# Performance work log

Hardware: AMD Instinct MI355X
Metric: run time of the kernel (lower is better)

## Reference

```python
import jax, jax.numpy as jnp
import numpy as np
import math

HEAD = 4
B, N, C = 8, 1024, 256


def setup_inputs() -> dict:
    key = jax.random.key(0)
    k1, k2, k3, k4, k5 = jax.random.split(key, 5)
    query = jax.random.normal(k1, (B, N, C), dtype=jnp.float32)
    keyt = jax.random.normal(k2, (B, N, C), dtype=jnp.float32)
    value = jax.random.normal(k3, (B, N, C), dtype=jnp.float32)
    mask = jax.random.randint(k4, (B, N, N), 0, 2).astype(bool)
    dis = jax.random.normal(k5, (B, N, N), dtype=jnp.float32)
    return {"query": query, "key": keyt, "value": value, "mask": mask, "dis": dis}


def reference(query, key, value, mask, dis):
    Bq, Nq, Cq = key.shape
    d = Cq // HEAD
    # split heads: [B,N,C] -> [h,B,N,d]
    q = query.reshape(Bq, Nq, HEAD, d).transpose(2, 0, 1, 3)
    k = key.reshape(Bq, Nq, HEAD, d).transpose(2, 0, 1, 3)
    v = value.reshape(Bq, Nq, HEAD, d).transpose(2, 0, 1, 3)
    # scores: [h,B,N,N]; note: dis added BEFORE scaling, as in the torch code
    scores = jnp.einsum('hbnd,hbmd->hbnm', q, k)
    scores = scores + dis[None]            # dis broadcasts over head dim
    scores = scores / math.sqrt(d)
    scores = jnp.where(mask[None], -jnp.inf, scores)
    p_attn = jax.nn.softmax(scores, axis=-1)
    out = jnp.einsum('hbnm,hbmd->hbnd', p_attn, v)  # [h,B,N,d]
    out = out.transpose(1, 2, 0, 3).reshape(Bq, Nq, Cq)
    return out, p_attn
```

## Files before the change

kernel.cpp:

```cpp
#include <hip/hip_runtime.h>
#include <math.h>

#define HEADS 4
#define BATCH 8
#define SEQ   1024
#define CH    256
#define DH    64
#define RB    16
#define MC    64
#define NTHR  256
#define SSTR  1032

typedef float  floatx4  __attribute__((ext_vector_type(4)));
typedef short  shortx8  __attribute__((ext_vector_type(8)));
typedef unsigned short ushortx4 __attribute__((ext_vector_type(4)));

__device__ __forceinline__ unsigned short f2bf(float f) {
    unsigned u = __float_as_uint(f);
    unsigned r = u + 0x7FFFu + ((u >> 16) & 1u);
    return (unsigned short)(r >> 16);
}
__device__ __forceinline__ float bf2f(unsigned short h) {
    return __uint_as_float(((unsigned)h) << 16);
}
__device__ __forceinline__ shortx8 pack8(float4 a, float4 b) {
    shortx8 r;
    r[0] = (short)f2bf(a.x); r[1] = (short)f2bf(a.y);
    r[2] = (short)f2bf(a.z); r[3] = (short)f2bf(a.w);
    r[4] = (short)f2bf(b.x); r[5] = (short)f2bf(b.y);
    r[6] = (short)f2bf(b.z); r[7] = (short)f2bf(b.w);
    return r;
}

__global__ void detect_mask_kernel(const unsigned char* __restrict__ mb,
                                   int* __restrict__ flag) {
    int t = threadIdx.x;
    int found = 0;
    for (int o = t * 64; o < t * 64 + 64; ++o)
        if ((o & 3) != 0 && mb[o] != 0) found = 1;
    unsigned long long ball = __ballot(found != 0);
    if (t == 0) flag[0] = (ball != 0ULL) ? 1 : 0;
}

__global__ __launch_bounds__(NTHR, 4)
void attn_mfma(const float* __restrict__ q, const float* __restrict__ k,
               const float* __restrict__ v, const void* __restrict__ maskp,
               const float* __restrict__ dis, float* __restrict__ out,
               float* __restrict__ pout, const int* __restrict__ flag)
{
    __shared__ unsigned short Sraw[RB][SSTR];
    __shared__ float invs[RB];

    const int t   = threadIdx.x;
    const int bid = blockIdx.x;
    const int nb  = bid & 63;
    const int hb  = bid >> 6;
    const int b   = hb & (BATCH - 1);
    const int h   = hb >> 3;
    const int n0  = nb * RB;
    const int fl  = flag[0];
    const unsigned char* mask8  = (const unsigned char*)maskp;
    const int*           mask32 = (const int*)maskp;

    const int lane = t & 63;
    const int w    = t >> 6;
    const int ln   = lane & 15;
    const int qd   = lane >> 4;

    const float* qrow = q + ((size_t)(b * SEQ + n0 + ln)) * CH + h * DH;
    shortx8 aq0, aq1;
    {
        float4 a0 = *(const float4*)(qrow + qd * 8);
        float4 a1 = *(const float4*)(qrow + qd * 8 + 4);
        float4 a2 = *(const float4*)(qrow + 32 + qd * 8);
        float4 a3 = *(const float4*)(qrow + 32 + qd * 8 + 4);
        aq0 = pack8(a0, a1);
        aq1 = pack8(a2, a3);
    }

    const float* kbase = k + ((size_t)(b * SEQ)) * CH + h * DH;
    const float* vbase = v + ((size_t)(b * SEQ)) * CH + h * DH;

    for (int mc = 0; mc < SEQ / MC; ++mc) {
        const int mg = mc * MC + w * 16 + ln;
        const float* krow = kbase + (size_t)mg * CH;
        float4 k0 = *(const float4*)(krow + qd * 8);
        float4 k1 = *(const float4*)(krow + qd * 8 + 4);
        float4 k2 = *(const float4*)(krow + 32 + qd * 8);
        float4 k3 = *(const float4*)(krow + 32 + qd * 8 + 4);
        const size_t dibase = ((size_t)(b * SEQ + n0 + qd * 4)) * SEQ + mg;
        float dv[4]; int mk[4];
        if (fl) {
            #pragma unroll
            for (int r = 0; r < 4; ++r) mk[r] = mask8[dibase + (size_t)r * SEQ];
        } else {
            #pragma unroll
            for (int r = 0; r < 4; ++r) mk[r] = mask32[dibase + (size_t)r * SEQ];
        }
        #pragma unroll
        for (int r = 0; r < 4; ++r) dv[r] = dis[dibase + (size_t)r * SEQ];

        shortx8 b0 = pack8(k0, k1), b1 = pack8(k2, k3);
        floatx4 acc = {0.f, 0.f, 0.f, 0.f};
        acc = __builtin_amdgcn_mfma_f32_16x16x32_bf16(aq0, b0, acc, 0, 0, 0);
        acc = __builtin_amdgcn_mfma_f32_16x16x32_bf16(aq1, b1, acc, 0, 0, 0);
        #pragma unroll
        for (int r = 0; r < 4; ++r) {
            float sc = mk[r] ? -INFINITY : (acc[r] + dv[r]) * 0.125f;
            Sraw[qd * 4 + r][mg] = f2bf(sc);
        }
    }
    __syncthreads();

    {
        const int r = t >> 4, l = t & 15;
        float mx = -INFINITY;
        #pragma unroll
        for (int j = 0; j < 8; ++j) {
            shortx8 sv = *(const shortx8*)&Sraw[r][j * 128 + l * 8];
            #pragma unroll
            for (int e = 0; e < 8; ++e) mx = fmaxf(mx, bf2f((unsigned short)sv[e]));
        }
        #pragma unroll
        for (int off = 8; off; off >>= 1) mx = fmaxf(mx, __shfl_xor(mx, off, 16));
        float sum = 0.f;
        #pragma unroll
        for (int j = 0; j < 8; ++j) {
            shortx8 sv = *(const shortx8*)&Sraw[r][j * 128 + l * 8];
            shortx8 ev;
            #pragma unroll
            for (int e = 0; e < 8; ++e) {
                float x = __expf(bf2f((unsigned short)sv[e]) - mx);
                sum += x;
                ev[e] = (short)f2bf(x);
            }
            *(shortx8*)&Sraw[r][j * 128 + l * 8] = ev;
        }
        #pragma unroll
        for (int off = 8; off; off >>= 1) sum += __shfl_xor(sum, off, 16);
        if (l == 0) invs[r] = 1.0f / sum;
    }
    __syncthreads();

    {
        float* prow = pout + ((size_t)((h * BATCH + b) * SEQ + n0)) * SEQ;
        #pragma unroll
        for (int i = 0; i < RB; ++i) {
            const float inv = invs[i];
            ushortx4 sp = *(const ushortx4*)&Sraw[i][t * 4];
            float4 pv = { bf2f(sp[0]) * inv, bf2f(sp[1]) * inv,
                          bf2f(sp[2]) * inv, bf2f(sp[3]) * inv };
            *(float4*)(prow + (size_t)i * SEQ + t * 4) = pv;
        }
    }

    floatx4 acco = {0.f, 0.f, 0.f, 0.f};
    for (int mc = 0; mc < SEQ / MC; ++mc) {
        #pragma unroll
        for (int s = 0; s < 2; ++s) {
            const int kb = mc * MC + s * 32 + qd * 8;
            float vv[8];
            #pragma unroll
            for (int j = 0; j < 8; ++j)
                vv[j] = vbase[(size_t)(kb + j) * CH + w * 16 + ln];
            shortx8 af = *(const shortx8*)&Sraw[ln][mc * MC + s * 32 + qd * 8];
            shortx8 bfv;
            #pragma unroll
            for (int j = 0; j < 8; ++j) bfv[j] = (short)f2bf(vv[j]);
            acco = __builtin_amdgcn_mfma_f32_16x16x32_bf16(af, bfv, acco, 0, 0, 0);
        }
    }
    #pragma unroll
    for (int r = 0; r < 4; ++r) {
        int row = qd * 4 + r;
        out[((size_t)(b * SEQ + n0 + row)) * CH + h * DH + w * 16 + ln]
            = acco[r] * invs[row];
    }
}

extern "C" void kernel_launch(void* const* d_in, const int* in_sizes, int n_in,
                              void* d_out, int out_size, void* d_ws, size_t ws_size,
                              hipStream_t stream) {
    const float* q    = (const float*)d_in[0];
    const float* k    = (const float*)d_in[1];
    const float* v    = (const float*)d_in[2];
    const void*  mask = d_in[3];
    const float* dis  = (const float*)d_in[4];
    float* out  = (float*)d_out;
    float* pout = out + (size_t)BATCH * SEQ * CH;
    int*   flag = (int*)d_ws;

    detect_mask_kernel<<<1, 64, 0, stream>>>((const unsigned char*)mask, flag);
    attn_mfma<<<HEADS * BATCH * (SEQ / RB), NTHR, 0, stream>>>(
        q, k, v, mask, dis, out, pout, flag);
}
```

Before: 315.1 us.

## Double threads per block, split PV over key halves, inline mask detection

Raises the block size from 256 to 512 threads. The score loop now covers 128 keys per iteration with 8 waves, and the softmax uses 32 lanes per row. The P@V stage splits the key range in half across two groups of waves, and the partial outputs are reduced through shared memory. The separate mask-format detection kernel is removed: each block samples the mask itself with a ballot, which saves a launch at the cost of a small redundant read in every block. The extra shared buffer and the higher launch-bounds target may limit occupancy or registers.

```diff
diff --git a/kernel.cpp b/kernel.cpp
--- a/kernel.cpp
+++ b/kernel.cpp
@@ -7,13 +7,11 @@
 #define CH    256
 #define DH    64
 #define RB    16
-#define MC    64
-#define NTHR  256
+#define NTHR  512
 #define SSTR  1032
 
 typedef float  floatx4  __attribute__((ext_vector_type(4)));
 typedef short  shortx8  __attribute__((ext_vector_type(8)));
-typedef unsigned short ushortx4 __attribute__((ext_vector_type(4)));
 
 __device__ __forceinline__ unsigned short f2bf(float f) {
     unsigned u = __float_as_uint(f);
@@ -32,23 +30,14 @@
     return r;
 }
 
-__global__ void detect_mask_kernel(const unsigned char* __restrict__ mb,
-                                   int* __restrict__ flag) {
-    int t = threadIdx.x;
-    int found = 0;
-    for (int o = t * 64; o < t * 64 + 64; ++o)
-        if ((o & 3) != 0 && mb[o] != 0) found = 1;
-    unsigned long long ball = __ballot(found != 0);
-    if (t == 0) flag[0] = (ball != 0ULL) ? 1 : 0;
-}
-
-__global__ __launch_bounds__(NTHR, 4)
+__global__ __launch_bounds__(NTHR, 8)
 void attn_mfma(const float* __restrict__ q, const float* __restrict__ k,
                const float* __restrict__ v, const void* __restrict__ maskp,
                const float* __restrict__ dis, float* __restrict__ out,
-               float* __restrict__ pout, const int* __restrict__ flag)
+               float* __restrict__ pout)
 {
     __shared__ unsigned short Sraw[RB][SSTR];
+    __shared__ float Opart[RB][65];
     __shared__ float invs[RB];
 
     const int t   = threadIdx.x;
@@ -58,14 +47,23 @@
     const int b   = hb & (BATCH - 1);
     const int h   = hb >> 3;
     const int n0  = nb * RB;
-    const int fl  = flag[0];
-    const unsigned char* mask8  = (const unsigned char*)maskp;
-    const int*           mask32 = (const int*)maskp;
 
     const int lane = t & 63;
     const int w    = t >> 6;
     const int ln   = lane & 15;
     const int qd   = lane >> 4;
+
+    int fl;
+    {
+        const unsigned* mw = (const unsigned*)maskp;
+        int found = 0;
+        #pragma unroll
+        for (int j = 0; j < 16; ++j)
+            if (mw[lane * 16 + j] & 0xFFFFFF00u) found = 1;
+        fl = (__ballot(found != 0) != 0ULL) ? 1 : 0;
+    }
+    const unsigned char* mask8  = (const unsigned char*)maskp;
+    const int*           mask32 = (const int*)maskp;
 
     const float* qrow = q + ((size_t)(b * SEQ + n0 + ln)) * CH + h * DH;
     shortx8 aq0, aq1;
@@ -81,24 +79,25 @@
     const float* kbase = k + ((size_t)(b * SEQ)) * CH + h * DH;
     const float* vbase = v + ((size_t)(b * SEQ)) * CH + h * DH;
 
-    for (int mc = 0; mc < SEQ / MC; ++mc) {
-        const int mg = mc * MC + w * 16 + ln;
+    #pragma unroll 2
+    for (int mc = 0; mc < 8; ++mc) {
+        const int mg = mc * 128 + w * 16 + ln;
+        const size_t dibase = ((size_t)(b * SEQ + n0 + qd * 4)) * SEQ + mg;
+        float dv[4]; int mk[4];
+        #pragma unroll
+        for (int r = 0; r < 4; ++r) dv[r] = dis[dibase + (size_t)r * SEQ];
+        if (fl) {
+            #pragma unroll
+            for (int r = 0; r < 4; ++r) mk[r] = mask8[dibase + (size_t)r * SEQ];
+        } else {
+            #pragma unroll
+            for (int r = 0; r < 4; ++r) mk[r] = mask32[dibase + (size_t)r * SEQ];
+        }
         const float* krow = kbase + (size_t)mg * CH;
         float4 k0 = *(const float4*)(krow + qd * 8);
         float4 k1 = *(const float4*)(krow + qd * 8 + 4);
         float4 k2 = *(const float4*)(krow + 32 + qd * 8);
         float4 k3 = *(const float4*)(krow + 32 + qd * 8 + 4);
-        const size_t dibase = ((size_t)(b * SEQ + n0 + qd * 4)) * SEQ + mg;
-        float dv[4]; int mk[4];
-        if (fl) {
-            #pragma unroll
-            for (int r = 0; r < 4; ++r) mk[r] = mask8[dibase + (size_t)r * SEQ];
-        } else {
-            #pragma unroll
-            for (int r = 0; r < 4; ++r) mk[r] = mask32[dibase + (size_t)r * SEQ];
-        }
-        #pragma unroll
-        for (int r = 0; r < 4; ++r) dv[r] = dis[dibase + (size_t)r * SEQ];
 
         shortx8 b0 = pack8(k0, k1), b1 = pack8(k2, k3);
         floatx4 acc = {0.f, 0.f, 0.f, 0.f};
@@ -113,20 +112,20 @@
     __syncthreads();
 
     {
-        const int r = t >> 4, l = t & 15;
+        const int r = t >> 5, l = t & 31;
         float mx = -INFINITY;
         #pragma unroll
-        for (int j = 0; j < 8; ++j) {
-            shortx8 sv = *(const shortx8*)&Sraw[r][j * 128 + l * 8];
+        for (int j = 0; j < 4; ++j) {
+            shortx8 sv = *(const shortx8*)&Sraw[r][j * 256 + l * 8];
             #pragma unroll
             for (int e = 0; e < 8; ++e) mx = fmaxf(mx, bf2f((unsigned short)sv[e]));
         }
         #pragma unroll
-        for (int off = 8; off; off >>= 1) mx = fmaxf(mx, __shfl_xor(mx, off, 16));
+        for (int off = 16; off; off >>= 1) mx = fmaxf(mx, __shfl_xor(mx, off, 32));
         float sum = 0.f;
         #pragma unroll
-        for (int j = 0; j < 8; ++j) {
-            shortx8 sv = *(const shortx8*)&Sraw[r][j * 128 + l * 8];
+        for (int j = 0; j < 4; ++j) {
+            shortx8 sv = *(const shortx8*)&Sraw[r][j * 256 + l * 8];
             shortx8 ev;
             #pragma unroll
             for (int e = 0; e < 8; ++e) {
@@ -134,10 +133,10 @@
                 sum += x;
                 ev[e] = (short)f2bf(x);
             }
-            *(shortx8*)&Sraw[r][j * 128 + l * 8] = ev;
-        }
-        #pragma unroll
-        for (int off = 8; off; off >>= 1) sum += __shfl_xor(sum, off, 16);
+            *(shortx8*)&Sraw[r][j * 256 + l * 8] = ev;
+        }
+        #pragma unroll
+        for (int off = 16; off; off >>= 1) sum += __shfl_xor(sum, off, 32);
         if (l == 0) invs[r] = 1.0f / sum;
     }
     __syncthreads();
@@ -147,34 +146,43 @@
         #pragma unroll
         for (int i = 0; i < RB; ++i) {
             const float inv = invs[i];
-            ushortx4 sp = *(const ushortx4*)&Sraw[i][t * 4];
-            float4 pv = { bf2f(sp[0]) * inv, bf2f(sp[1]) * inv,
-                          bf2f(sp[2]) * inv, bf2f(sp[3]) * inv };
-            *(float4*)(prow + (size_t)i * SEQ + t * 4) = pv;
-        }
-    }
-
+            unsigned pk = *(const unsigned*)&Sraw[i][t * 2];
+            float2 pv = { bf2f((unsigned short)(pk & 0xFFFFu)) * inv,
+                          bf2f((unsigned short)(pk >> 16)) * inv };
+            *(float2*)(prow + (size_t)i * SEQ + t * 2) = pv;
+        }
+    }
+
+    const int hm = w >> 2;
+    const int c  = (w & 3) * 16;
     floatx4 acco = {0.f, 0.f, 0.f, 0.f};
-    for (int mc = 0; mc < SEQ / MC; ++mc) {
+    for (int mc = 0; mc < 8; ++mc) {
         #pragma unroll
         for (int s = 0; s < 2; ++s) {
-            const int kb = mc * MC + s * 32 + qd * 8;
+            const int kb = hm * 512 + mc * 64 + s * 32 + qd * 8;
             float vv[8];
             #pragma unroll
             for (int j = 0; j < 8; ++j)
-                vv[j] = vbase[(size_t)(kb + j) * CH + w * 16 + ln];
-            shortx8 af = *(const shortx8*)&Sraw[ln][mc * MC + s * 32 + qd * 8];
+                vv[j] = vbase[(size_t)(kb + j) * CH + c + ln];
+            shortx8 af = *(const shortx8*)&Sraw[ln][kb];
             shortx8 bfv;
             #pragma unroll
             for (int j = 0; j < 8; ++j) bfv[j] = (short)f2bf(vv[j]);
             acco = __builtin_amdgcn_mfma_f32_16x16x32_bf16(af, bfv, acco, 0, 0, 0);
         }
     }
-    #pragma unroll
-    for (int r = 0; r < 4; ++r) {
-        int row = qd * 4 + r;
-        out[((size_t)(b * SEQ + n0 + row)) * CH + h * DH + w * 16 + ln]
-            = acco[r] * invs[row];
+    if (hm == 1) {
+        #pragma unroll
+        for (int r = 0; r < 4; ++r) Opart[qd * 4 + r][c + ln] = acco[r];
+    }
+    __syncthreads();
+    if (hm == 0) {
+        #pragma unroll
+        for (int r = 0; r < 4; ++r) {
+            int row = qd * 4 + r;
+            out[((size_t)(b * SEQ + n0 + row)) * CH + h * DH + c + ln]
+                = (acco[r] + Opart[row][c + ln]) * invs[row];
+        }
     }
 }
 
@@ -188,9 +196,8 @@
     const float* dis  = (const float*)d_in[4];
     float* out  = (float*)d_out;
     float* pout = out + (size_t)BATCH * SEQ * CH;
-    int*   flag = (int*)d_ws;
-
-    detect_mask_kernel<<<1, 64, 0, stream>>>((const unsigned char*)mask, flag);
+    (void)d_ws; (void)ws_size;
+
     attn_mfma<<<HEADS * BATCH * (SEQ / RB), NTHR, 0, stream>>>(
-        q, k, v, mask, dis, out, pout, flag);
-}
+        q, k, v, mask, dis, out, pout);
+}
```

After: 310.7 us. Within noise of the previous version (-1.4%).
